# Performance work log

Measured on AMD Instinct MI355X. Metric: run time of the kernel, lower is better.

The kernel has to match this reference:

```python
import jax, jax.numpy as jnp
import numpy as np

N_NODES = 50000


def setup_inputs() -> dict:
    key = jax.random.key(0)
    k1, k2, k3 = jax.random.split(key, 3)
    x = jax.random.normal(k1, (N_NODES, 128), dtype=jnp.float32)
    edge_index = jax.random.randint(k2, (2, 800000), 0, N_NODES, dtype=jnp.int64)
    weight = jax.random.normal(k3, (128, 128), dtype=jnp.float32) * (1.0 / np.sqrt(128))
    bias = jnp.zeros((128,), dtype=jnp.float32)
    return {"x": x, "edge_index": edge_index, "weight": weight, "bias": bias}


def reference(x, edge_index, weight, bias):
    # GCNConv (PyG defaults): add self-loops, sym-normalize, linear, scatter-add, bias; then ReLU.
    N = x.shape[0]
    self_loops = jnp.arange(N, dtype=edge_index.dtype)
    row = jnp.concatenate([edge_index[0], self_loops])  # source nodes [E+N]
    col = jnp.concatenate([edge_index[1], self_loops])  # target nodes [E+N]

    # degree over targets (edge weights are all ones), includes self-loops -> deg >= 1
    deg = jax.ops.segment_sum(jnp.ones_like(col, dtype=x.dtype), col, num_segments=N)
    dinv = jax.lax.rsqrt(deg)
    norm = dinv[row] * dinv[col]  # [E+N]

    h = x @ weight  # [N, nhid] linear transform before propagation
    msgs = h[row] * norm[:, None]  # gather + scale, [E+N, nhid]
    out = jax.ops.segment_sum(msgs, col, num_segments=N) + bias  # scatter-add aggregate
    return jax.nn.relu(out)
```

## Files before the change

### kernel.cpp

```cpp
#include <hip/hip_runtime.h>

#define NFEAT 128
#define CAP 64
#define NROLE 4
#define CHUNK 2048

typedef __attribute__((ext_vector_type(8))) short short8;
typedef __attribute__((ext_vector_type(4))) float f32x4;
typedef __attribute__((ext_vector_type(4))) float f32x4v;
typedef __attribute__((ext_vector_type(2))) float f32x2v;
typedef __attribute__((ext_vector_type(4))) int i32x4;

__device__ inline short f2bf(float f) {
    unsigned u = __builtin_bit_cast(unsigned, f);
    u += 0x7FFFu + ((u >> 16) & 1u);
    return (short)(u >> 16);
}
__device__ inline float bf2f(unsigned short u) {
    return __builtin_bit_cast(float, ((unsigned)u) << 16);
}

__global__ void prep_kernel(const float* __restrict__ W, unsigned short* __restrict__ Wt,
                            unsigned int* __restrict__ cnt, int N) {
    int i = blockIdx.x * 256 + threadIdx.x;
    if (i < N) cnt[i] = 0u;
    if (i < NFEAT * NFEAT) {
        int k = i >> 7, n = i & 127;
        Wt[n * NFEAT + k] = (unsigned short)f2bf(W[k * NFEAT + n]);
    }
}

__global__ void __launch_bounds__(256)
gemm_countfill_kernel(const float* __restrict__ x,
                      const unsigned short* __restrict__ Wt,
                      unsigned short* __restrict__ h, int N, int gb,
                      const int* __restrict__ row, const int* __restrict__ col,
                      int E, unsigned int* __restrict__ cnt,
                      unsigned short* __restrict__ bucket) {
    __shared__ unsigned short tile[4][16][136];
    int bid = blockIdx.x;

    if (bid >= gb) {
        int k = bid - gb;
        int role = bid & (NROLE - 1);
        int q = k >> 2;
        int rlo = (int)((long long)N * role / NROLE);
        int rhi = (int)((long long)N * (role + 1) / NROLE);
        int ebase = q * CHUNK + (int)threadIdx.x * 4;
        #pragma unroll
        for (int half = 0; half < 2; ++half) {
            int e = ebase + half * 1024;
            if (e + 3 < E) {
                i32x4 c4 = *(const i32x4*)(col + e);
                bool m0 = (c4[0] >= rlo) & (c4[0] < rhi);
                bool m1 = (c4[1] >= rlo) & (c4[1] < rhi);
                bool m2 = (c4[2] >= rlo) & (c4[2] < rhi);
                bool m3 = (c4[3] >= rlo) & (c4[3] < rhi);
                if (m0 | m1 | m2 | m3) {
                    i32x4 r4 = *(const i32x4*)(row + e);
                    #pragma unroll
                    for (int u = 0; u < 4; ++u) {
                        int c = c4[u];
                        if (c >= rlo && c < rhi) {
                            unsigned int t = atomicAdd(&cnt[c], 1u);
                            if (t < CAP) bucket[(size_t)c * CAP + t] = (unsigned short)r4[u];
                        }
                    }
                }
            }
        }
        return;
    }

    int wave = threadIdx.x >> 6;
    int lane = threadIdx.x & 63;
    int li = lane & 15;
    int kg = lane >> 4;
    int m0 = bid * 64 + wave * 16;
    int arow = m0 + li;
    int srow = (arow < N) ? arow : (N - 1);

    f32x4 acc[8];
    #pragma unroll
    for (int nt = 0; nt < 8; ++nt) acc[nt] = (f32x4){0.f, 0.f, 0.f, 0.f};

    #pragma unroll
    for (int ks = 0; ks < 4; ++ks) {
        const f32x4v* xp = (const f32x4v*)(x + (size_t)srow * NFEAT + ks * 32 + kg * 8);
        f32x4v f0 = __builtin_nontemporal_load(xp);
        f32x4v f1 = __builtin_nontemporal_load(xp + 1);
        short8 a;
        a[0] = f2bf(f0.x); a[1] = f2bf(f0.y); a[2] = f2bf(f0.z); a[3] = f2bf(f0.w);
        a[4] = f2bf(f1.x); a[5] = f2bf(f1.y); a[6] = f2bf(f1.z); a[7] = f2bf(f1.w);
        #pragma unroll
        for (int nt = 0; nt < 8; ++nt) {
            short8 b = *(const short8*)(Wt + (size_t)(nt * 16 + li) * NFEAT + ks * 32 + kg * 8);
            acc[nt] = __builtin_amdgcn_mfma_f32_16x16x32_bf16(a, b, acc[nt], 0, 0, 0);
        }
    }

    #pragma unroll
    for (int r = 0; r < 4; ++r) {
        #pragma unroll
        for (int nt = 0; nt < 8; ++nt)
            tile[wave][kg * 4 + r][nt * 16 + li] = (unsigned short)f2bf(acc[nt][r]);
    }
    __syncthreads();

    int rr = lane >> 2;
    int orow = m0 + rr;
    #pragma unroll
    for (int cc = 0; cc < 4; ++cc) {
        int chunk = cc * 4 + (lane & 3);
        if (orow < N) {
            short8 v = *(const short8*)&tile[wave][rr][chunk * 8];
            __builtin_nontemporal_store(v, (short8*)(h + (size_t)orow * NFEAT + chunk * 8));
        }
    }
}

__global__ void aggregate_kernel(const unsigned short* __restrict__ h,
                                 const unsigned short* __restrict__ bucket,
                                 const unsigned int* __restrict__ cnt,
                                 const float* __restrict__ bias,
                                 float* __restrict__ out, int N) {
    int wid = threadIdx.x >> 6;
    int lane = threadIdx.x & 63;
    int c = blockIdx.x * 4 + wid;
    if (c >= N) return;
    int grp = lane >> 4;
    int li = lane & 15;
    int col0 = li * 8;
    int n = (int)cnt[c];
    float dc = rsqrtf((float)(n + 1));
    if (n > CAP) n = CAP;

    int myidx = (lane < n) ? (int)bucket[(size_t)c * CAP + lane] : c;
    float mydr = (lane < n) ? rsqrtf((float)(cnt[myidx] + 1u)) : 0.f;

    float acc[8];
    if (grp == 0) {
        short8 v = *(const short8*)(h + (size_t)c * NFEAT + col0);
        #pragma unroll
        for (int i = 0; i < 8; ++i) acc[i] = bf2f((unsigned short)v[i]) * dc;
    } else {
        #pragma unroll
        for (int i = 0; i < 8; ++i) acc[i] = 0.f;
    }

    for (int j = 0; j < n; j += 16) {
        int idx[4];
        float dr[4];
        short8 v[4];
        #pragma unroll
        for (int k = 0; k < 4; ++k) {
            int e = j + k * 4 + grp;
            idx[k] = __shfl(myidx, e, 64);
            dr[k] = __shfl(mydr, e, 64);
        }
        #pragma unroll
        for (int k = 0; k < 4; ++k)
            v[k] = *(const short8*)(h + (size_t)idx[k] * NFEAT + col0);
        #pragma unroll
        for (int k = 0; k < 4; ++k) {
            #pragma unroll
            for (int i = 0; i < 8; ++i) acc[i] += bf2f((unsigned short)v[k][i]) * dr[k];
        }
    }

    #pragma unroll
    for (int i = 0; i < 8; ++i) {
        acc[i] += __shfl_xor(acc[i], 16, 64);
        acc[i] += __shfl_xor(acc[i], 32, 64);
    }

    float a0, a1;
    switch (grp) {
        case 0: a0 = acc[0]; a1 = acc[1]; break;
        case 1: a0 = acc[2]; a1 = acc[3]; break;
        case 2: a0 = acc[4]; a1 = acc[5]; break;
        default: a0 = acc[6]; a1 = acc[7]; break;
    }
    const float2* bp = (const float2*)(bias + col0 + grp * 2);
    float2 b = *bp;
    f32x2v o;
    o.x = fmaxf(a0 * dc + b.x, 0.f);
    o.y = fmaxf(a1 * dc + b.y, 0.f);
    __builtin_nontemporal_store(o, (f32x2v*)(out + (size_t)c * NFEAT + col0 + grp * 2));
}

extern "C" void kernel_launch(void* const* d_in, const int* in_sizes, int n_in,
                              void* d_out, int out_size, void* d_ws, size_t ws_size,
                              hipStream_t stream) {
    const float* x    = (const float*)d_in[0];
    const int*   ei   = (const int*)d_in[1];
    const float* W    = (const float*)d_in[2];
    const float* bias = (const float*)d_in[3];
    float* out = (float*)d_out;

    int N = in_sizes[0] / NFEAT;
    int E = in_sizes[1] / 2;
    const int* row = ei;
    const int* col = ei + E;

    char* ws = (char*)d_ws;
    size_t o = 0;
    unsigned int*   cnt    = (unsigned int*)(ws + o);   o += (size_t)N * 4;
    unsigned short* Wt     = (unsigned short*)(ws + o); o += (size_t)NFEAT * NFEAT * 2;
    unsigned short* bucket = (unsigned short*)(ws + o); o += (size_t)N * CAP * 2;
    unsigned short* h      = (unsigned short*)(ws + o);

    int nb = (N + 255) / 256;
    int gb = (N + 63) / 64;
    int per_role = (E + CHUNK - 1) / CHUNK;
    int cb = NROLE * per_role;

    prep_kernel<<<nb, 256, 0, stream>>>(W, Wt, cnt, N);
    gemm_countfill_kernel<<<gb + cb, 256, 0, stream>>>(x, Wt, h, N, gb,
                                                       row, col, E, cnt, bucket);
    aggregate_kernel<<<(N + 3) / 4, 256, 0, stream>>>(h, bucket, cnt, bias, out, N);
}
```

Baseline: 104.1 us.

## Merge count-fill and GEMM into persistent blocks with atomic ticket tile scheduling

Replaces the split grid, where separate blocks did either the GEMM or the edge bucketing, with a fixed grid of 2048 blocks. Each block first bucket-fills one edge chunk for one of 8 node-range roles, then pulls GEMM row tiles from a global atomic ticket counter until none remain. This aims to overlap the irregular atomic scatter with the MFMA GEMM inside each block and to balance load dynamically. The cost is extra per-tile syncs and ticket atomics, and the wider role split means col is reread more times. Edge loads become nontemporal.

Measured after the change: 143.9 us. +38.3%, slower.

```diff
diff --git a/kernel.cpp b/kernel.cpp
--- a/kernel.cpp
+++ b/kernel.cpp
@@ -2,8 +2,9 @@
 
 #define NFEAT 128
 #define CAP 64
-#define NROLE 4
-#define CHUNK 2048
+#define NROLE 8
+#define CFB 2048
+#define ECHUNK 4096
 
 typedef __attribute__((ext_vector_type(8))) short short8;
 typedef __attribute__((ext_vector_type(4))) float f32x4;
@@ -21,9 +22,11 @@
 }
 
 __global__ void prep_kernel(const float* __restrict__ W, unsigned short* __restrict__ Wt,
-                            unsigned int* __restrict__ cnt, int N) {
+                            unsigned int* __restrict__ cnt, unsigned int* __restrict__ ticket,
+                            int N) {
     int i = blockIdx.x * 256 + threadIdx.x;
     if (i < N) cnt[i] = 0u;
+    if (i == 0) *ticket = 0u;
     if (i < NFEAT * NFEAT) {
         int k = i >> 7, n = i & 127;
         Wt[n * NFEAT + k] = (unsigned short)f2bf(W[k * NFEAT + n]);
@@ -31,90 +34,101 @@
 }
 
 __global__ void __launch_bounds__(256)
-gemm_countfill_kernel(const float* __restrict__ x,
-                      const unsigned short* __restrict__ Wt,
-                      unsigned short* __restrict__ h, int N, int gb,
-                      const int* __restrict__ row, const int* __restrict__ col,
-                      int E, unsigned int* __restrict__ cnt,
-                      unsigned short* __restrict__ bucket) {
+hybrid_kernel(const float* __restrict__ x,
+              const unsigned short* __restrict__ Wt,
+              unsigned short* __restrict__ h, int N, int gb,
+              const int* __restrict__ row, const int* __restrict__ col,
+              int E, unsigned int* __restrict__ cnt,
+              unsigned short* __restrict__ bucket,
+              unsigned int* __restrict__ ticket) {
     __shared__ unsigned short tile[4][16][136];
+    __shared__ int tkt;
     int bid = blockIdx.x;
 
-    if (bid >= gb) {
-        int k = bid - gb;
+    {
         int role = bid & (NROLE - 1);
-        int q = k >> 2;
-        int rlo = (int)((long long)N * role / NROLE);
-        int rhi = (int)((long long)N * (role + 1) / NROLE);
-        int ebase = q * CHUNK + (int)threadIdx.x * 4;
-        #pragma unroll
-        for (int half = 0; half < 2; ++half) {
-            int e = ebase + half * 1024;
-            if (e + 3 < E) {
-                i32x4 c4 = *(const i32x4*)(col + e);
-                bool m0 = (c4[0] >= rlo) & (c4[0] < rhi);
-                bool m1 = (c4[1] >= rlo) & (c4[1] < rhi);
-                bool m2 = (c4[2] >= rlo) & (c4[2] < rhi);
-                bool m3 = (c4[3] >= rlo) & (c4[3] < rhi);
-                if (m0 | m1 | m2 | m3) {
-                    i32x4 r4 = *(const i32x4*)(row + e);
-                    #pragma unroll
-                    for (int u = 0; u < 4; ++u) {
-                        int c = c4[u];
-                        if (c >= rlo && c < rhi) {
-                            unsigned int t = atomicAdd(&cnt[c], 1u);
-                            if (t < CAP) bucket[(size_t)c * CAP + t] = (unsigned short)r4[u];
+        int q = bid >> 3;
+        int base = q * ECHUNK;
+        if (base < E) {
+            int rlo = (int)((long long)N * role / NROLE);
+            int rhi = (int)((long long)N * (role + 1) / NROLE);
+            #pragma unroll
+            for (int i = 0; i < 4; ++i) {
+                int e = base + (i * 256 + (int)threadIdx.x) * 4;
+                if (e < E) {
+                    i32x4 c4 = __builtin_nontemporal_load((const i32x4*)(col + e));
+                    bool m0 = (c4[0] >= rlo) & (c4[0] < rhi);
+                    bool m1 = (c4[1] >= rlo) & (c4[1] < rhi);
+                    bool m2 = (c4[2] >= rlo) & (c4[2] < rhi);
+                    bool m3 = (c4[3] >= rlo) & (c4[3] < rhi);
+                    if (m0 | m1 | m2 | m3) {
+                        i32x4 r4 = __builtin_nontemporal_load((const i32x4*)(row + e));
+                        #pragma unroll
+                        for (int u = 0; u < 4; ++u) {
+                            int c = c4[u];
+                            if (c >= rlo && c < rhi) {
+                                unsigned int t = atomicAdd(&cnt[c], 1u);
+                                if (t < CAP) bucket[(size_t)c * CAP + t] = (unsigned short)r4[u];
+                            }
                         }
                     }
                 }
             }
         }
-        return;
     }
 
     int wave = threadIdx.x >> 6;
     int lane = threadIdx.x & 63;
     int li = lane & 15;
     int kg = lane >> 4;
-    int m0 = bid * 64 + wave * 16;
-    int arow = m0 + li;
-    int srow = (arow < N) ? arow : (N - 1);
-
-    f32x4 acc[8];
-    #pragma unroll
-    for (int nt = 0; nt < 8; ++nt) acc[nt] = (f32x4){0.f, 0.f, 0.f, 0.f};
-
-    #pragma unroll
-    for (int ks = 0; ks < 4; ++ks) {
-        const f32x4v* xp = (const f32x4v*)(x + (size_t)srow * NFEAT + ks * 32 + kg * 8);
-        f32x4v f0 = __builtin_nontemporal_load(xp);
-        f32x4v f1 = __builtin_nontemporal_load(xp + 1);
-        short8 a;
-        a[0] = f2bf(f0.x); a[1] = f2bf(f0.y); a[2] = f2bf(f0.z); a[3] = f2bf(f0.w);
-        a[4] = f2bf(f1.x); a[5] = f2bf(f1.y); a[6] = f2bf(f1.z); a[7] = f2bf(f1.w);
-        #pragma unroll
-        for (int nt = 0; nt < 8; ++nt) {
-            short8 b = *(const short8*)(Wt + (size_t)(nt * 16 + li) * NFEAT + ks * 32 + kg * 8);
-            acc[nt] = __builtin_amdgcn_mfma_f32_16x16x32_bf16(a, b, acc[nt], 0, 0, 0);
-        }
-    }
-
-    #pragma unroll
-    for (int r = 0; r < 4; ++r) {
-        #pragma unroll
-        for (int nt = 0; nt < 8; ++nt)
-            tile[wave][kg * 4 + r][nt * 16 + li] = (unsigned short)f2bf(acc[nt][r]);
-    }
-    __syncthreads();
-
-    int rr = lane >> 2;
-    int orow = m0 + rr;
-    #pragma unroll
-    for (int cc = 0; cc < 4; ++cc) {
-        int chunk = cc * 4 + (lane & 3);
-        if (orow < N) {
-            short8 v = *(const short8*)&tile[wave][rr][chunk * 8];
-            __builtin_nontemporal_store(v, (short8*)(h + (size_t)orow * NFEAT + chunk * 8));
+
+    while (true) {
+        __syncthreads();
+        if (threadIdx.x == 0) tkt = (int)atomicAdd(ticket, 1u);
+        __syncthreads();
+        int t = tkt;
+        if (t >= gb) break;
+
+        int m0 = t * 64 + wave * 16;
+        int arow = m0 + li;
+        int srow = (arow < N) ? arow : (N - 1);
+
+        f32x4 acc[8];
+        #pragma unroll
+        for (int nt = 0; nt < 8; ++nt) acc[nt] = (f32x4){0.f, 0.f, 0.f, 0.f};
+
+        #pragma unroll
+        for (int ks = 0; ks < 4; ++ks) {
+            const f32x4v* xp = (const f32x4v*)(x + (size_t)srow * NFEAT + ks * 32 + kg * 8);
+            f32x4v f0 = __builtin_nontemporal_load(xp);
+            f32x4v f1 = __builtin_nontemporal_load(xp + 1);
+            short8 a;
+            a[0] = f2bf(f0.x); a[1] = f2bf(f0.y); a[2] = f2bf(f0.z); a[3] = f2bf(f0.w);
+            a[4] = f2bf(f1.x); a[5] = f2bf(f1.y); a[6] = f2bf(f1.z); a[7] = f2bf(f1.w);
+            #pragma unroll
+            for (int nt = 0; nt < 8; ++nt) {
+                short8 b = *(const short8*)(Wt + (size_t)(nt * 16 + li) * NFEAT + ks * 32 + kg * 8);
+                acc[nt] = __builtin_amdgcn_mfma_f32_16x16x32_bf16(a, b, acc[nt], 0, 0, 0);
+            }
+        }
+
+        #pragma unroll
+        for (int r = 0; r < 4; ++r) {
+            #pragma unroll
+            for (int nt = 0; nt < 8; ++nt)
+                tile[wave][kg * 4 + r][nt * 16 + li] = (unsigned short)f2bf(acc[nt][r]);
+        }
+        __syncthreads();
+
+        int rr = lane >> 2;
+        int orow = m0 + rr;
+        #pragma unroll
+        for (int cc = 0; cc < 4; ++cc) {
+            int chunk = cc * 4 + (lane & 3);
+            if (orow < N) {
+                short8 v = *(const short8*)&tile[wave][rr][chunk * 8];
+                __builtin_nontemporal_store(v, (short8*)(h + (size_t)orow * NFEAT + chunk * 8));
+            }
         }
     }
 }
@@ -206,17 +220,16 @@
     char* ws = (char*)d_ws;
     size_t o = 0;
     unsigned int*   cnt    = (unsigned int*)(ws + o);   o += (size_t)N * 4;
+    unsigned int*   ticket = (unsigned int*)(ws + o);   o += 16;
     unsigned short* Wt     = (unsigned short*)(ws + o); o += (size_t)NFEAT * NFEAT * 2;
     unsigned short* bucket = (unsigned short*)(ws + o); o += (size_t)N * CAP * 2;
     unsigned short* h      = (unsigned short*)(ws + o);
 
     int nb = (N + 255) / 256;
     int gb = (N + 63) / 64;
-    int per_role = (E + CHUNK - 1) / CHUNK;
-    int cb = NROLE * per_role;
-
-    prep_kernel<<<nb, 256, 0, stream>>>(W, Wt, cnt, N);
-    gemm_countfill_kernel<<<gb + cb, 256, 0, stream>>>(x, Wt, h, N, gb,
-                                                       row, col, E, cnt, bucket);
+
+    prep_kernel<<<nb, 256, 0, stream>>>(W, Wt, cnt, ticket, N);
+    hybrid_kernel<<<CFB, 256, 0, stream>>>(x, Wt, h, N, gb,
+                                           row, col, E, cnt, bucket, ticket);
     aggregate_kernel<<<(N + 3) / 4, 256, 0, stream>>>(h, bucket, cnt, bias, out, N);
 }
```
